# Performance work log

Hardware: AMD Instinct MI355X
Metric: run time of the kernel (lower is better)

## Reference

```python
import math
import jax, jax.numpy as jnp
import numpy as np

# ---------------- static config ----------------
L_MAX = 3
DIM = (L_MAX + 1) ** 2            # 16 = dim of 0e+1o+2e+3o
N_NODES = 8000
N_EDGES = 128000                  # avg 16 neighbors / node
F = 32                            # num_features (irrep multiplicity)
S = 10                            # num_species
NB = 8                            # num bessel basis fns
HID = 64                          # radial MLP hidden width
RD_HID = 16                       # readout MLP hidden (16x0e)
R_MAX = 5.0
AVG_NEIGH = 16.0
MEAN, STD = -1.5, 2.0
E0 = -10.0                        # atomic energy offset per node

_f = math.factorial

def _sl(l):
    return slice(l * l, (l + 1) * (l + 1))

# ---------------- real Clebsch-Gordan / Wigner-3j tables ----------------
def _su2_cg(j1, j2, j3):
    C = np.zeros((2 * j1 + 1, 2 * j2 + 1, 2 * j3 + 1))
    for m1 in range(-j1, j1 + 1):
        for m2 in range(-j2, j2 + 1):
            m3 = m1 + m2
            if abs(m3) > j3:
                continue
            pref = (2 * j3 + 1) * _f(j3 + j1 - j2) * _f(j3 - j1 + j2) * _f(j1 + j2 - j3) / _f(j1 + j2 + j3 + 1)
            pref *= _f(j3 + m3) * _f(j3 - m3) * _f(j1 - m1) * _f(j1 + m1) * _f(j2 - m2) * _f(j2 + m2)
            pref = math.sqrt(pref)
            s = 0.0
            for k in range(max(0, j2 - j3 - m1, j1 - j3 + m2), min(j1 + j2 - j3, j1 - m1, j2 + m2) + 1):
                s += (-1) ** k / (_f(k) * _f(j1 + j2 - j3 - k) * _f(j1 - m1 - k) * _f(j2 + m2 - k) * _f(j3 - j2 + m1 + k) * _f(j3 - j1 - m2 + k))
            C[j1 + m1, j2 + m2, j3 + m3] = pref * s
    return C

def _q_r2c(l):
    # complex <- real spherical-harmonic change of basis (e3nn convention)
    q = np.zeros((2 * l + 1, 2 * l + 1), dtype=complex)
    for m in range(-l, 0):
        q[l + m, l + abs(m)] = 1 / math.sqrt(2)
        q[l + m, l - abs(m)] = -1j / math.sqrt(2)
    q[l, l] = 1.0
    for m in range(1, l + 1):
        q[l + m, l + abs(m)] = (-1) ** m / math.sqrt(2)
        q[l + m, l - abs(m)] = 1j * (-1) ** m / math.sqrt(2)
    return (-1j) ** l * q

def _w3j(l1, l2, l3):
    C = _su2_cg(l1, l2, l3).astype(complex)
    C = np.einsum('abc,ai,bj,ck->ijk', C, _q_r2c(l1), _q_r2c(l2), np.conj(_q_r2c(l3)))
    assert np.abs(C.imag).max() < 1e-8
    return np.real(C)

PATHS = [(l1, l2, l3) for l1 in range(L_MAX + 1) for l2 in range(L_MAX + 1)
         for l3 in range(L_MAX + 1) if abs(l1 - l2) <= l3 <= l1 + l2]
NP_PATHS = len(PATHS)  # 34 CG paths
_W3J_NP = {p: _w3j(*p) for p in PATHS}
W3J = {p: jnp.asarray(v, dtype=jnp.float32) for p, v in _W3J_NP.items()}

def _sh_scales():
    # constants making recursively-built SH component-normalized (|Y_l|^2 = 2l+1)
    v = np.array([0.2, -0.6, 0.7]); v = v / np.linalg.norm(v)
    ys = {1: math.sqrt(3.0) * v}
    sc = {}
    for l in range(2, L_MAX + 1):
        t = np.einsum('abc,a,b->c', _W3J_NP[(l - 1, 1, l)], ys[l - 1], ys[1])
        sc[l] = math.sqrt(2 * l + 1) / np.linalg.norm(t)
        ys[l] = sc[l] * t
    return sc
SH_SCALE = _sh_scales()

# ---------------- equivariant building blocks ----------------
def spherical_harmonics(vectors):
    r = jnp.linalg.norm(vectors, axis=-1, keepdims=True)
    u = vectors / jnp.maximum(r, 1e-9)
    y1 = math.sqrt(3.0) * u
    Y = jnp.concatenate([jnp.ones_like(u[:, :1]), y1], axis=-1)
    prev = y1
    for l in range(2, L_MAX + 1):
        cur = SH_SCALE[l] * jnp.einsum('abc,ea,eb->ec', W3J[(l - 1, 1, l)], prev, y1)
        Y = jnp.concatenate([Y, cur], axis=-1)
        prev = cur
    return Y  # [E, 16]

def radial_embedding(r):
    # Bessel basis * polynomial envelope (RadialEmbeddingBlock)
    x = r / R_MAX
    n = jnp.arange(1, NB + 1, dtype=r.dtype)
    b = math.sqrt(2.0 / R_MAX) * jnp.sin(jnp.pi * x[:, None] * n[None, :]) / jnp.maximum(r, 1e-9)[:, None]
    p = 5.0
    env = 1 - (p + 1) * (p + 2) / 2 * x ** p + p * (p + 2) * x ** (p + 1) - p * (p + 1) / 2 * x ** (p + 2)
    env = jnp.where(x < 1.0, env, 0.0)
    return b * env[:, None]  # [E, NB]

def _lin(x, w):
    # e3nn Linear: per-l channel mixing. x [N,F,DIM], w [L_MAX+1,F,F]
    return jnp.concatenate([jnp.einsum('nfa,fg->nga', x[:, :, _sl(l)], w[l]) for l in range(L_MAX + 1)], axis=-1)

def _tp_edge(xs, Y, rw):
    # radially-weighted CG tensor product of node feats with edge SH (InteractionBlock core)
    out = jnp.zeros_like(xs)
    for p, (l1, l2, l3) in enumerate(PATHS):
        t = jnp.einsum('abc,efa,eb->efc', W3J[(l1, l2, l3)], xs[:, :, _sl(l1)], Y[:, _sl(l2)])
        out = out.at[:, :, _sl(l3)].add(rw[:, p, :, None] * t)
    return out

def _tp_node(x, y):
    # channel-wise symmetric CG product (EquivariantProductBasisBlock contraction)
    out = jnp.zeros_like(x)
    for (l1, l2, l3) in PATHS:
        t = jnp.einsum('abc,nfa,nfb->nfc', W3J[(l1, l2, l3)], x[:, :, _sl(l1)], y[:, :, _sl(l2)])
        out = out.at[:, :, _sl(l3)].add(t / math.sqrt(2 * l3 + 1))
    return out

# ---------------- inputs ----------------
def setup_inputs() -> dict:
    key = jax.random.key(0)
    ks = iter(jax.random.split(key, 40))
    def nrm(shape, fan):
        return jax.random.normal(next(ks), shape, dtype=jnp.float32) / math.sqrt(fan)
    inp = {}
    inp['vectors'] = jax.random.normal(next(ks), (N_EDGES, 3), dtype=jnp.float32) * 1.5
    inp['node_z'] = jax.random.randint(next(ks), (N_NODES,), 0, S)
    inp['senders'] = jax.random.randint(next(ks), (N_EDGES,), 0, N_NODES)
    inp['receivers'] = jax.random.randint(next(ks), (N_EDGES,), 0, N_NODES)
    inp['embed'] = nrm((S, F), 1)
    for i in (0, 1):
        inp['r%d_w0' % i] = nrm((NB, HID), NB)
        inp['r%d_w1' % i] = nrm((HID, HID), HID)
        inp['r%d_w2' % i] = nrm((HID, NP_PATHS * F), HID)
        inp['up%d' % i] = nrm((L_MAX + 1, F, F), F)
        inp['post%d' % i] = nrm((L_MAX + 1, F, F), F)
        inp['pb%d' % i] = nrm((S, 3, F), 1)
        inp['pblin%d' % i] = nrm((L_MAX + 1, F, F), F)
    inp['sel0'] = nrm((S, L_MAX + 1, F, F), F)
    inp['ro0'] = nrm((F, 1), F)
    inp['res1'] = nrm((S, F, F), F)
    inp['ro1_a'] = nrm((F, RD_HID), F)
    inp['ro1_b'] = nrm((RD_HID, 1), RD_HID)
    return inp

# ---------------- forward ----------------
def reference(vectors, node_z, senders, receivers, embed,
              r0_w0, r0_w1, r0_w2, up0, post0, pb0, pblin0, sel0, ro0,
              r1_w0, r1_w1, r1_w2, up1, post1, pb1, pblin1, res1, ro1_a, ro1_b):
    N = node_z.shape[0]
    r = jnp.linalg.norm(vectors, axis=-1)
    Y = spherical_harmonics(vectors)
    rad = radial_embedding(r)
    # node embedding: scalars only
    feats = jnp.zeros((N, F, DIM), vectors.dtype).at[:, :, 0].set(embed[node_z])

    def interaction(feats, w0, w1, w2, wup, wpost):
        h = _lin(feats, wup)
        rw = (jax.nn.silu(jax.nn.silu(rad @ w0) @ w1) @ w2).reshape(-1, NP_PATHS, F)
        msgs = _tp_edge(h[senders], Y, rw)
        agg = jax.ops.segment_sum(msgs, receivers, num_segments=N) / AVG_NEIGH
        return _lin(agg, wpost)

    def product_basis(A, wpb, wlin, z):
        B2 = _tp_node(A, A)           # correlation order 2
        B3 = _tp_node(B2, A)          # correlation order 3
        w = wpb[z]                     # [N,3,F] per-species contraction weights
        out = w[:, 0, :, None] * A + w[:, 1, :, None] * B2 + w[:, 2, :, None] * B3
        return _lin(out, wlin)

    # ---- layer 0: selector tensor product, linear readout ----
    h = interaction(feats, r0_w0, r0_w1, r0_w2, up0, post0)
    wz = sel0[node_z]  # FullyConnectedTensorProduct with one-hot species == per-species linear
    h = jnp.concatenate([jnp.einsum('nfa,nfg->nga', h[:, :, _sl(l)], wz[:, l]) for l in range(L_MAX + 1)], axis=-1)
    feats = product_basis(h, pb0, pblin0, node_z)
    e0 = (feats[:, :, 0] @ ro0)[:, 0]

    # ---- layer 1 (last): residual to scalars, nonlinear readout ----
    resid = jnp.einsum('nf,nfg->ng', feats[:, :, 0], res1[node_z])
    h = interaction(feats, r1_w0, r1_w1, r1_w2, up1, post1)
    h = product_basis(h, pb1, pblin1, node_z)
    sc = h[:, :, 0] + resid  # last-layer target irreps = F x 0e
    e1 = (jax.nn.silu(sc @ ro1_a) @ ro1_b)[:, 0]

    node_energies = MEAN + STD * (e0 + e1) + E0
    return jnp.sum(node_energies)
```

## Files before the change

kernel.cpp:

```cpp
#include <hip/hip_runtime.h>
#include <math.h>

#define NF 32
#define NPATHS 34

typedef __attribute__((ext_vector_type(8))) short bf16x8;
typedef __attribute__((ext_vector_type(4))) float f32x4;
typedef __attribute__((ext_vector_type(2))) float f32x2;

__device__ __forceinline__ unsigned short f2bf(float v){
  unsigned u = __float_as_uint(v);
  u += 0x7fffu + ((u>>16)&1u);
  return (unsigned short)(u>>16);
}
__device__ __forceinline__ float bf2f(unsigned short h){
  return __uint_as_float(((unsigned)h)<<16);
}

struct PathTab { int l1[NPATHS]; int l2[NPATHS]; int l3[NPATHS]; };
constexpr PathTab mkpaths(){
  PathTab t{}; int n=0;
  for(int a=0;a<=3;a++)for(int b=0;b<=3;b++)for(int c=0;c<=3;c++){
    int lo = a>b ? a-b : b-a;
    if(c>=lo && c<=a+b){ t.l1[n]=a; t.l2[n]=b; t.l3[n]=c; n++; }
  }
  return t;
}
constexpr PathTab PT = mkpaths();

struct FactT { double v[22]; };
constexpr FactT mkfactT(){ FactT f{}; f.v[0]=1.0; for(int i=1;i<22;i++) f.v[i]=f.v[i-1]*(double)i; return f; }
constexpr FactT FT = mkfactT();
constexpr double cfact(int n){ return FT.v[n]; }

constexpr double csqrt(double x){
  if(x<=0.0) return 0.0;
  double g = x<1.0 ? 1.0 : x;
  for(int i=0;i<40;i++) g=0.5*(g+x/g);
  return g;
}

constexpr double su2cg(int j1,int j2,int j3,int m1,int m2){
  int m3=m1+m2;
  if(m3<-j3||m3>j3) return 0.0;
  double pref = (double)(2*j3+1)*cfact(j3+j1-j2)*cfact(j3-j1+j2)*cfact(j1+j2-j3)/cfact(j1+j2+j3+1);
  pref *= cfact(j3+m3)*cfact(j3-m3)*cfact(j1-m1)*cfact(j1+m1)*cfact(j2-m2)*cfact(j2+m2);
  pref = csqrt(pref);
  int k0=0; if(j2-j3-m1>k0)k0=j2-j3-m1; if(j1-j3+m2>k0)k0=j1-j3+m2;
  int k1=j1+j2-j3; if(j1-m1<k1)k1=j1-m1; if(j2+m2<k1)k1=j2+m2;
  double s=0.0;
  for(int k=k0;k<=k1;k++){
    double d = cfact(k)*cfact(j1+j2-j3-k)*cfact(j1-m1-k)*cfact(j2+m2-k)*cfact(j3-j2+m1+k)*cfact(j3-j1-m2+k);
    s += (k&1)? -1.0/d : 1.0/d;
  }
  return pref*s;
}

struct ccd { double x, y; };
constexpr ccd cqval(int l,int r,int col){
  const double is2 = 0.70710678118654752440;
  double re=0.0, im=0.0;
  if (r<l){ if (col==2*l-r) re=is2; else if (col==r) im=-is2; }
  else if (r==l){ if (col==l) re=1.0; }
  else { double s = ((r-l)&1)? -1.0:1.0;
         if (col==r) re=s*is2; else if (col==2*l-r) im=s*is2; }
  ccd v{re,im};
  switch(l&3){
    case 1: return ccd{ v.y, -v.x };
    case 2: return ccd{-v.x, -v.y };
    case 3: return ccd{-v.y,  v.x };
    default: return v;
  }
}

constexpr double w3entry(int l1,int l2,int l3,int i,int j,int k){
  double re=0.0;
  for(int a=0;a<2*l1+1;a++){
    ccd qa=cqval(l1,a,i); if(qa.x==0.0&&qa.y==0.0) continue;
    for(int b=0;b<2*l2+1;b++){
      ccd qb=cqval(l2,b,j); if(qb.x==0.0&&qb.y==0.0) continue;
      int m1=a-l1, m2=b-l2, m3=m1+m2;
      if(m3<-l3||m3>l3) continue;
      int c=m3+l3;
      double cg=su2cg(l1,l2,l3,m1,m2); if(cg==0.0) continue;
      ccd qc=cqval(l3,c,k); qc.y=-qc.y;
      if(qc.x==0.0&&qc.y==0.0) continue;
      ccd ab{qa.x*qb.x-qa.y*qb.y, qa.x*qb.y+qa.y*qb.x};
      re += cg*(ab.x*qc.x - ab.y*qc.y);
    }
  }
  return re;
}

template<int L1,int L2,int L3> struct W3Arr { float v[(2*L1+1)*(2*L2+1)*(2*L3+1)]; };
template<int L1,int L2,int L3> constexpr W3Arr<L1,L2,L3> mkW3(double scale){
  W3Arr<L1,L2,L3> r{};
  for(int i=0;i<2*L1+1;i++)
    for(int j=0;j<2*L2+1;j++)
      for(int k=0;k<2*L3+1;k++)
        r.v[(i*(2*L2+1)+j)*(2*L3+1)+k] = (float)(w3entry(L1,L2,L3,i,j,k)*scale);
  return r;
}
template<int L1,int L2,int L3> constexpr W3Arr<L1,L2,L3> W3V = mkW3<L1,L2,L3>(1.0);
template<int L1,int L2,int L3> constexpr W3Arr<L1,L2,L3> W3N = mkW3<L1,L2,L3>(1.0/csqrt(2.0*L3+1.0));

struct SCt { double sc2, sc3; };
constexpr SCt mksc(){
  double v0=0.2,v1=-0.6,v2=0.7;
  double nv=csqrt(v0*v0+v1*v1+v2*v2);
  double s3=csqrt(3.0);
  double y1[3]={s3*v0/nv, s3*v1/nv, s3*v2/nv};
  double t2[5]={0,0,0,0,0}; double n2=0.0;
  for(int c=0;c<5;c++){
    double s=0.0;
    for(int a=0;a<3;a++)for(int b=0;b<3;b++) s += w3entry(1,1,2,a,b,c)*y1[a]*y1[b];
    t2[c]=s; n2+=s*s;
  }
  double sc2=csqrt(5.0)/csqrt(n2);
  double y2[5]={sc2*t2[0],sc2*t2[1],sc2*t2[2],sc2*t2[3],sc2*t2[4]};
  double n3=0.0;
  for(int c=0;c<7;c++){
    double s=0.0;
    for(int a=0;a<5;a++)for(int b=0;b<3;b++) s += w3entry(2,1,3,a,b,c)*y2[a]*y1[b];
    n3+=s*s;
  }
  double sc3=csqrt(7.0)/csqrt(n3);
  return SCt{sc2,sc3};
}
constexpr SCt SCV = mksc();

template<bool NORM,int l1,int l2,int l3,int A,int B,int C>
__device__ __forceinline__ void w3term(const float* __restrict__ x, const float* __restrict__ y,
                                       float rv, float* __restrict__ acc){
  constexpr float w = NORM ? W3N<l1,l2,l3>.v[(A*(2*l2+1)+B)*(2*l3+1)+C]
                           : W3V<l1,l2,l3>.v[(A*(2*l2+1)+B)*(2*l3+1)+C];
  if constexpr (w!=0.0f)
    acc[l3*l3+C] = fmaf(w, x[l1*l1+A]*y[l2*l2+B]*rv, acc[l3*l3+C]);
}
template<bool NORM,int l1,int l2,int l3,int A,int B,int C>
__device__ __forceinline__ void w3loopC(const float* x,const float* y,float rv,float* acc){
  if constexpr (C<2*l3+1){
    w3term<NORM,l1,l2,l3,A,B,C>(x,y,rv,acc);
    w3loopC<NORM,l1,l2,l3,A,B,C+1>(x,y,rv,acc);
  }
}
template<bool NORM,int l1,int l2,int l3,int A,int B>
__device__ __forceinline__ void w3loopB(const float* x,const float* y,float rv,float* acc){
  if constexpr (B<2*l2+1){
    w3loopC<NORM,l1,l2,l3,A,B,0>(x,y,rv,acc);
    w3loopB<NORM,l1,l2,l3,A,B+1>(x,y,rv,acc);
  }
}
template<bool NORM,int l1,int l2,int l3,int A>
__device__ __forceinline__ void w3loopA(const float* x,const float* y,float rv,float* acc){
  if constexpr (A<2*l1+1){
    w3loopB<NORM,l1,l2,l3,A,0>(x,y,rv,acc);
    w3loopA<NORM,l1,l2,l3,A+1>(x,y,rv,acc);
  }
}

template<int P>
__device__ __forceinline__ void tpn_paths(const float* x,const float* y,float* o){
  if constexpr (P<NPATHS){
    constexpr int l1=PT.l1[P], l2=PT.l2[P], l3=PT.l3[P];
    w3loopA<true,l1,l2,l3,0>(x,y,1.0f,o);
    tpn_paths<P+1>(x,y,o);
  }
}

__device__ __forceinline__ float tpn_scalar(const float* x,const float* y){
  float o[1]={0.f};
  w3loopA<true,0,0,0,0>(x,y,1.0f,o);
  w3loopA<true,1,1,0,0>(x,y,1.0f,o);
  w3loopA<true,2,2,0,0>(x,y,1.0f,o);
  w3loopA<true,3,3,0,0>(x,y,1.0f,o);
  return o[0];
}

template<int l1,int l2,int l3,int A,int B>
constexpr bool anyNZ(){
  for(int c=0;c<2*l3+1;c++)
    if(W3V<l1,l2,l3>.v[(A*(2*l2+1)+B)*(2*l3+1)+c]!=0.0f) return true;
  return false;
}
template<int l1,int l2,int l3,int A,int B,int C>
__device__ __forceinline__ void w3C2(const f32x2 p, f32x2* __restrict__ S){
  constexpr float w = W3V<l1,l2,l3>.v[(A*(2*l2+1)+B)*(2*l3+1)+C];
  if constexpr (w!=0.0f) S[C] = p*w + S[C];
  if constexpr (C+1<2*l3+1) w3C2<l1,l2,l3,A,B,C+1>(p,S);
}
template<int l1,int l2,int l3,int A,int B>
__device__ __forceinline__ void w3B2(const f32x2* __restrict__ x,const f32x2* __restrict__ y,
                                     f32x2* __restrict__ S){
  if constexpr (anyNZ<l1,l2,l3,A,B>()){
    f32x2 p = x[l1*l1+A]*y[l2*l2+B];
    w3C2<l1,l2,l3,A,B,0>(p,S);
  }
  if constexpr (B+1<2*l2+1) w3B2<l1,l2,l3,A,B+1>(x,y,S);
}
template<int l1,int l2,int l3,int A>
__device__ __forceinline__ void w3A2(const f32x2* __restrict__ x,const f32x2* __restrict__ y,
                                     f32x2* __restrict__ S){
  w3B2<l1,l2,l3,A,0>(x,y,S);
  if constexpr (A+1<2*l1+1) w3A2<l1,l2,l3,A+1>(x,y,S);
}
template<bool L0,int P>
__device__ __forceinline__ void tp2(const f32x2* __restrict__ x,const f32x2* __restrict__ y,
                                    const unsigned short* __restrict__ rpA,
                                    const unsigned short* __restrict__ rpB,
                                    f32x2* __restrict__ acc){
  if constexpr (P<NPATHS){
    constexpr int l1=PT.l1[P], l2=PT.l2[P], l3=PT.l3[P];
    if constexpr (!(L0 && l1!=0)){
      f32x2 S[2*l3+1];
      #pragma unroll
      for(int c=0;c<2*l3+1;c++) S[c]=(f32x2){0.f,0.f};
      w3A2<l1,l2,l3,0>(x,y,S);
      f32x2 rv = { bf2f(rpA[P]), bf2f(rpB[P]) };
      #pragma unroll
      for(int c=0;c<2*l3+1;c++) acc[l3*l3+c] = rv*S[c] + acc[l3*l3+c];
    }
    tp2<L0,P+1>(x,y,rpA,rpB,acc);
  }
}

__global__ __launch_bounds__(256) void k_count(
    const int* __restrict__ rcv, int* __restrict__ deg, int E)
{
  int e=blockIdx.x*256+threadIdx.x;
  if(e>=E) return;
  atomicAdd(&deg[rcv[e]],1);
}

#define SCAN_PER 32
__global__ __launch_bounds__(1024) void k_scan(
    const int* __restrict__ deg, int* __restrict__ row,
    int* __restrict__ cur, int N)
{
  __shared__ int part[1024];
  int t=threadIdx.x;
  int per=(N+1023)/1024; if(per>SCAN_PER) per=SCAN_PER;
  int base=t*per;
  int loc[SCAN_PER];
  int s=0;
  for(int i=0;i<per;i++){ int idx=base+i; int v=(idx<N)? deg[idx]:0; loc[i]=s; s+=v; }
  part[t]=s;
  __syncthreads();
  for(int off=1;off<1024;off<<=1){
    int v=(t>=off)? part[t-off]:0;
    __syncthreads();
    part[t]+=v;
    __syncthreads();
  }
  int ex=(t==0)?0:part[t-1];
  for(int i=0;i<per;i++){
    int idx=base+i;
    if(idx<N){ int r=ex+loc[i]; row[idx]=r; cur[idx]=r; }
  }
  if(t==1023) row[N]=part[1023];
}

__global__ __launch_bounds__(256) void k_fill(
    const int* __restrict__ rcv, int* __restrict__ cur,
    int* __restrict__ eid, int E)
{
  int e=blockIdx.x*256+threadIdx.x;
  if(e>=E) return;
  int pos=atomicAdd(&cur[rcv[e]],1);
  eid[pos]=e;
}

__global__ __launch_bounds__(256) void k_edge_setup(
    const float* __restrict__ vec, const int* __restrict__ snd,
    const int* __restrict__ eid, float* __restrict__ Y,
    float* __restrict__ rad, int* __restrict__ snd_s, int E)
{
  int j = blockIdx.x*256+threadIdx.x;
  if (j>=E) return;
  int e = eid[j];
  snd_s[j]=snd[e];
  float vx=vec[3*e], vy=vec[3*e+1], vz=vec[3*e+2];
  float r=sqrtf(vx*vx+vy*vy+vz*vz);
  float inv=1.0f/fmaxf(r,1e-9f);
  float y[16];
  y[0]=1.0f;
  const float s3=1.7320508075688772f;
  y[1]=s3*vx*inv; y[2]=s3*vy*inv; y[3]=s3*vz*inv;
  constexpr float sc2=(float)SCV.sc2, sc3=(float)SCV.sc3;
  {
    float t[16];
    #pragma unroll
    for(int c=0;c<16;c++) t[c]=0.f;
    w3loopA<false,1,1,2,0>(y,y,1.0f,t);
    #pragma unroll
    for(int c=0;c<5;c++) y[4+c]=sc2*t[4+c];
    w3loopA<false,2,1,3,0>(y,y,1.0f,t);
    #pragma unroll
    for(int c=0;c<7;c++) y[9+c]=sc3*t[9+c];
  }
  float4* Yp=(float4*)(Y+(size_t)j*16);
  Yp[0]=make_float4(y[0],y[1],y[2],y[3]);
  Yp[1]=make_float4(y[4],y[5],y[6],y[7]);
  Yp[2]=make_float4(y[8],y[9],y[10],y[11]);
  Yp[3]=make_float4(y[12],y[13],y[14],y[15]);
  float x = r*0.2f;
  float env=0.f;
  if (x<1.0f){
    float x2=x*x; float x4=x2*x2; float x5=x4*x;
    env = 1.0f - 21.0f*x5 + 35.0f*x5*x - 15.0f*x5*x2;
  }
  const float cb = 0.632455532033675866f;
  float base = inv*env*cb;
  #pragma unroll
  for(int n=1;n<=8;n++)
    rad[(size_t)j*8 + n-1] = base*sinf(3.14159265358979323846f * x * (float)n);
}

__global__ __launch_bounds__(256) void k_embed16(
    const float* __restrict__ embed, const float* __restrict__ up0,
    const int* __restrict__ z, unsigned short* __restrict__ hl16, int N)
{
  int t=blockIdx.x*256+threadIdx.x;
  int n=t>>5, g=t&31;
  if(n>=N) return;
  const float* ep=embed+z[n]*32;
  float a=0.f;
  #pragma unroll 8
  for(int f=0;f<32;f++) a=fmaf(ep[f],up0[(f<<5)+g],a);
  bf16x8 o0={(short)f2bf(a),0,0,0,0,0,0,0};
  bf16x8 o1={0,0,0,0,0,0,0,0};
  bf16x8* op=(bf16x8*)(hl16+(size_t)n*512+g*16);
  op[0]=o0; op[1]=o1;
}

__global__ __launch_bounds__(256) void k_radial(
    const float* __restrict__ rad, const float* __restrict__ w0,
    const float* __restrict__ w1, unsigned short* __restrict__ hid, int E)
{
  __shared__ float w0s[8*64];
  __shared__ float w1s[64*64];
  int tid=threadIdx.x;
  for(int i=tid;i<512;i+=256) w0s[i]=w0[i];
  for(int i=tid;i<4096;i+=256) w1s[i]=w1[i];
  __syncthreads();
  int e=blockIdx.x*256+tid;
  if(e>=E) return;
  const float4* rp=(const float4*)(rad+(size_t)e*8);
  float4 ra=rp[0], rb=rp[1];
  float rv[8]={ra.x,ra.y,ra.z,ra.w,rb.x,rb.y,rb.z,rb.w};
  float h1[64];
  #pragma unroll 8
  for(int j=0;j<64;j++){
    float a=0.f;
    #pragma unroll
    for(int i=0;i<8;i++) a=fmaf(rv[i],w0s[i*64+j],a);
    h1[j]=a/(1.f+__expf(-a));
  }
  unsigned short* hp = hid+(size_t)e*64;
  #pragma unroll 4
  for(int j=0;j<64;j++){
    float a=0.f;
    #pragma unroll
    for(int i=0;i<64;i++) a=fmaf(h1[i],w1s[i*64+j],a);
    hp[j]=f2bf(a/(1.f+__expf(-a)));
  }
}

__global__ __launch_bounds__(256) void k_prep(
    const float* __restrict__ w2a, const float* __restrict__ w2b,
    unsigned short* __restrict__ ta, unsigned short* __restrict__ tb,
    const float* __restrict__ post0, const float* __restrict__ sel0,
    float* __restrict__ comb)
{
  int t=blockIdx.x*256+threadIdx.x;
  const int C2=2*1088*64;
  if(t<C2){
    const float* src = (t<1088*64)? w2a : w2b;
    unsigned short* dst = (t<1088*64)? ta : tb;
    int u = (t<1088*64)? t : t-1088*64;
    int c=u>>6, k=u&63;
    dst[(size_t)c*64+k]=f2bf(src[(size_t)k*1088+c]);
  } else {
    int u=t-C2;
    if(u<10*4096){
      int z=u>>12, r=u&4095;
      int l=r>>10, e=(r>>5)&31, g=r&31;
      const float* pp=post0+l*1024+e*32;
      const float* sp=sel0+(size_t)z*4096+l*1024;
      float a=0.f;
      #pragma unroll 8
      for(int f=0;f<32;f++) a=fmaf(pp[f], sp[f*32+g], a);
      comb[(size_t)z*4096 + l*1024 + e*32 + g]=a;
    }
  }
}

template<bool L0>
__global__ __launch_bounds__(256,3) void k_tp_fused(
    const unsigned short* __restrict__ hlin, const float* __restrict__ Y,
    const unsigned short* __restrict__ hid, const unsigned short* __restrict__ w2t,
    const int* __restrict__ snd_s, unsigned short* __restrict__ msgs,
    int eb, int ecnt)
{
  constexpr int NT  = L0 ? 8 : 68;
  constexpr int FS  = L0 ? 4 : 36;
  constexpr int ROW = 32*FS + 4;
  __shared__ unsigned short rws[16*ROW] __attribute__((aligned(16)));
  int tid=threadIdx.x;
  int lane=tid&63, wave=tid>>6;
  int m16=lane&15, quad=lane>>4;
  int el0=blockIdx.x*16;
  int f=tid&31;
  int hb=(tid>>5)&1;
  int le0 = wave + hb*8;
  int le1 = le0 + 4;
  int elA = el0 + le0, elB = el0 + le1;
  bool okA = elA<ecnt, okB = elB<ecnt;
  int sA = okA ? snd_s[eb+elA] : 0;
  int sB = okB ? snd_s[eb+elB] : 0;
  {
    const unsigned short* Ab = hid + (size_t)el0*64;
    bf16x8 a0 = *(const bf16x8*)(Ab + m16*64 + quad*8);
    bf16x8 a1 = *(const bf16x8*)(Ab + m16*64 + 32 + quad*8);
    #pragma unroll 4
    for(int nt=wave; nt<NT; nt+=4){
      int col = nt*16 + m16;
      bf16x8 b0 = *(const bf16x8*)(w2t + (size_t)col*64 + quad*8);
      bf16x8 b1 = *(const bf16x8*)(w2t + (size_t)col*64 + 32 + quad*8);
      f32x4 acc = (f32x4){0.f,0.f,0.f,0.f};
      acc = __builtin_amdgcn_mfma_f32_16x16x32_bf16(a0,b0,acc,0,0,0);
      acc = __builtin_amdgcn_mfma_f32_16x16x32_bf16(a1,b1,acc,0,0,0);
      int fo=(col&31)*FS + (col>>5);
      #pragma unroll
      for(int r=0;r<4;r++)
        rws[(quad*4+r)*ROW + fo] = f2bf(acc[r]);
    }
  }
  __syncthreads();
  if(!okA) return;
  int jA = eb+elA;
  int jB = okB ? eb+elB : jA;
  const unsigned short* rpA = rws + le0*ROW + f*FS;
  const unsigned short* rpB = rws + le1*ROW + f*FS;
  f32x2 hs[16];
  if constexpr (L0){
    const unsigned short* hA = hlin + (size_t)sA*512 + f*16;
    const unsigned short* hB = hlin + (size_t)sB*512 + f*16;
    hs[0] = (f32x2){ bf2f(hA[0]), bf2f(hB[0]) };
  } else {
    const bf16x8* hA = (const bf16x8*)(hlin + (size_t)sA*512 + f*16);
    const bf16x8* hB = (const bf16x8*)(hlin + (size_t)sB*512 + f*16);
    bf16x8 ha0=hA[0], ha1=hA[1], hb0=hB[0], hb1=hB[1];
    #pragma unroll
    for(int c=0;c<8;c++){
      hs[c]   = (f32x2){ bf2f((unsigned short)ha0[c]), bf2f((unsigned short)hb0[c]) };
      hs[8+c] = (f32x2){ bf2f((unsigned short)ha1[c]), bf2f((unsigned short)hb1[c]) };
    }
  }
  f32x2 yv[16];
  {
    const float4* yA=(const float4*)(Y+(size_t)jA*16);
    const float4* yB=(const float4*)(Y+(size_t)jB*16);
    float4 a0=yA[0],a1=yA[1],a2=yA[2],a3=yA[3];
    float4 b0=yB[0],b1=yB[1],b2=yB[2],b3=yB[3];
    yv[0]=(f32x2){a0.x,b0.x}; yv[1]=(f32x2){a0.y,b0.y}; yv[2]=(f32x2){a0.z,b0.z}; yv[3]=(f32x2){a0.w,b0.w};
    yv[4]=(f32x2){a1.x,b1.x}; yv[5]=(f32x2){a1.y,b1.y}; yv[6]=(f32x2){a1.z,b1.z}; yv[7]=(f32x2){a1.w,b1.w};
    yv[8]=(f32x2){a2.x,b2.x}; yv[9]=(f32x2){a2.y,b2.y}; yv[10]=(f32x2){a2.z,b2.z}; yv[11]=(f32x2){a2.w,b2.w};
    yv[12]=(f32x2){a3.x,b3.x}; yv[13]=(f32x2){a3.y,b3.y}; yv[14]=(f32x2){a3.z,b3.z}; yv[15]=(f32x2){a3.w,b3.w};
  }
  f32x2 acc[16];
  #pragma unroll
  for(int c=0;c<16;c++) acc[c]=(f32x2){0.f,0.f};
  tp2<L0,0>(hs,yv,rpA,rpB,acc);
  {
    bf16x8 m0, m1;
    #pragma unroll
    for(int c=0;c<8;c++){
      m0[c]=(short)f2bf(acc[c].x*0.0625f);
      m1[c]=(short)f2bf(acc[8+c].x*0.0625f);
    }
    bf16x8* mp=(bf16x8*)(msgs+(size_t)elA*512+f*16);
    mp[0]=m0; mp[1]=m1;
  }
  if(okB){
    bf16x8 m0, m1;
    #pragma unroll
    for(int c=0;c<8;c++){
      m0[c]=(short)f2bf(acc[c].y*0.0625f);
      m1[c]=(short)f2bf(acc[8+c].y*0.0625f);
    }
    bf16x8* mp=(bf16x8*)(msgs+(size_t)elB*512+f*16);
    mp[0]=m0; mp[1]=m1;
  }
}

template<bool INIT>
__global__ __launch_bounds__(256) void k_seg_sum(
    const unsigned short* __restrict__ msgs, const int* __restrict__ row,
    float* __restrict__ agg, int eb, int ecnt, int N)
{
  int t=blockIdx.x*256+threadIdx.x;
  int n=t>>6, q=t&63;
  if(n>=N) return;
  int lo=row[n], hi=row[n+1];
  int a0 = lo>eb ? lo : eb;
  int a1e = eb+ecnt;
  int a1 = hi<a1e ? hi : a1e;
  if(!INIT && a0>=a1) return;
  float s[8];
  #pragma unroll
  for(int i=0;i<8;i++) s[i]=0.f;
  for(int j=a0;j<a1;j++){
    bf16x8 v=*(const bf16x8*)(msgs+(size_t)(j-eb)*512+q*8);
    #pragma unroll
    for(int i=0;i<8;i++) s[i]+=bf2f((unsigned short)v[i]);
  }
  float4* a0p=(float4*)(agg+(size_t)n*512+q*8);
  if(INIT){
    a0p[0]=make_float4(s[0],s[1],s[2],s[3]);
    a0p[1]=make_float4(s[4],s[5],s[6],s[7]);
  } else {
    float4 o0=a0p[0], o1=a0p[1];
    o0.x+=s[0]; o0.y+=s[1]; o0.z+=s[2]; o0.w+=s[3];
    o1.x+=s[4]; o1.y+=s[5]; o1.z+=s[6]; o1.w+=s[7];
    a0p[0]=o0; a0p[1]=o1;
  }
}

__global__ __launch_bounds__(256) void k_node0(
    const float* __restrict__ agg, const float* __restrict__ combw,
    const float* __restrict__ pb0, const float* __restrict__ pblin0,
    const float* __restrict__ ro0, const float* __restrict__ res1,
    const float* __restrict__ up1, const int* __restrict__ z,
    float* __restrict__ e0, float* __restrict__ resid,
    unsigned short* __restrict__ hl16, int N)
{
  __shared__ float sh1[8*512] __attribute__((aligned(16)));
  __shared__ float sh2[8*512] __attribute__((aligned(16)));
  int tid=threadIdx.x;
  int n0=tid>>5, g=tid&31;
  int n=blockIdx.x*8+n0;
  bool act=(n<N);
  int zz = act? z[n] : 0;
  if(act){
    const float* wp = combw + (size_t)zz*4096;
    const float* ip = agg + (size_t)n*512;
    float A[16];
    #pragma unroll
    for(int c=0;c<16;c++) A[c]=0.f;
    #pragma unroll 8
    for(int f=0;f<NF;f++){
      const float4* xp=(const float4*)(ip+f*16);
      float4 x0=xp[0],x1=xp[1],x2=xp[2],x3=xp[3];
      float w0v=wp[(f<<5)+g],w1v=wp[1024+(f<<5)+g],w2v=wp[2048+(f<<5)+g],w3v=wp[3072+(f<<5)+g];
      A[0]=fmaf(x0.x,w0v,A[0]);  A[1]=fmaf(x0.y,w1v,A[1]);  A[2]=fmaf(x0.z,w1v,A[2]);  A[3]=fmaf(x0.w,w1v,A[3]);
      A[4]=fmaf(x1.x,w2v,A[4]);  A[5]=fmaf(x1.y,w2v,A[5]);  A[6]=fmaf(x1.z,w2v,A[6]);  A[7]=fmaf(x1.w,w2v,A[7]);
      A[8]=fmaf(x2.x,w2v,A[8]);  A[9]=fmaf(x2.y,w3v,A[9]);  A[10]=fmaf(x2.z,w3v,A[10]);A[11]=fmaf(x2.w,w3v,A[11]);
      A[12]=fmaf(x3.x,w3v,A[12]);A[13]=fmaf(x3.y,w3v,A[13]);A[14]=fmaf(x3.z,w3v,A[14]);A[15]=fmaf(x3.w,w3v,A[15]);
    }
    float B2[16],B3[16];
    #pragma unroll
    for(int c=0;c<16;c++){ B2[c]=0.f; B3[c]=0.f; }
    tpn_paths<0>(A,A,B2);
    tpn_paths<0>(B2,A,B3);
    float wa=pb0[zz*96+g], wb=pb0[zz*96+32+g], wc=pb0[zz*96+64+g];
    #pragma unroll
    for(int c=0;c<16;c++) sh1[n0*512+g*16+c]=wa*A[c]+wb*B2[c]+wc*B3[c];
  }
  __syncthreads();
  if(act){
    float ft[16];
    #pragma unroll
    for(int c=0;c<16;c++) ft[c]=0.f;
    const float* wp=pblin0;
    #pragma unroll 8
    for(int f=0;f<NF;f++){
      const float4* xp=(const float4*)(sh1+n0*512+f*16);
      float4 x0=xp[0],x1=xp[1],x2=xp[2],x3=xp[3];
      float w0v=wp[(f<<5)+g],w1v=wp[1024+(f<<5)+g],w2v=wp[2048+(f<<5)+g],w3v=wp[3072+(f<<5)+g];
      ft[0]=fmaf(x0.x,w0v,ft[0]);  ft[1]=fmaf(x0.y,w1v,ft[1]);  ft[2]=fmaf(x0.z,w1v,ft[2]);  ft[3]=fmaf(x0.w,w1v,ft[3]);
      ft[4]=fmaf(x1.x,w2v,ft[4]);  ft[5]=fmaf(x1.y,w2v,ft[5]);  ft[6]=fmaf(x1.z,w2v,ft[6]);  ft[7]=fmaf(x1.w,w2v,ft[7]);
      ft[8]=fmaf(x2.x,w2v,ft[8]);  ft[9]=fmaf(x2.y,w3v,ft[9]);  ft[10]=fmaf(x2.z,w3v,ft[10]);ft[11]=fmaf(x2.w,w3v,ft[11]);
      ft[12]=fmaf(x3.x,w3v,ft[12]);ft[13]=fmaf(x3.y,w3v,ft[13]);ft[14]=fmaf(x3.z,w3v,ft[14]);ft[15]=fmaf(x3.w,w3v,ft[15]);
    }
    #pragma unroll
    for(int c=0;c<16;c++) sh2[n0*512+g*16+c]=ft[c];
  }
  __syncthreads();
  if(act){
    const float* wp=res1+(size_t)zz*1024;
    float a=0.f;
    #pragma unroll 8
    for(int f=0;f<32;f++) a=fmaf(sh2[n0*512+f*16], wp[(f<<5)+g], a);
    resid[(size_t)n*32+g]=a;
    if(g==0){
      float b=0.f;
      #pragma unroll 8
      for(int f=0;f<32;f++) b=fmaf(sh2[n0*512+f*16], ro0[f], b);
      e0[n]=b;
    }
    float acc[16];
    #pragma unroll
    for(int c=0;c<16;c++) acc[c]=0.f;
    const float* wp2=up1;
    #pragma unroll 8
    for(int f=0;f<NF;f++){
      const float4* xp=(const float4*)(sh2+n0*512+f*16);
      float4 x0=xp[0],x1=xp[1],x2=xp[2],x3=xp[3];
      float w0v=wp2[(f<<5)+g],w1v=wp2[1024+(f<<5)+g],w2v=wp2[2048+(f<<5)+g],w3v=wp2[3072+(f<<5)+g];
      acc[0]=fmaf(x0.x,w0v,acc[0]);  acc[1]=fmaf(x0.y,w1v,acc[1]);  acc[2]=fmaf(x0.z,w1v,acc[2]);  acc[3]=fmaf(x0.w,w1v,acc[3]);
      acc[4]=fmaf(x1.x,w2v,acc[4]);  acc[5]=fmaf(x1.y,w2v,acc[5]);  acc[6]=fmaf(x1.z,w2v,acc[6]);  acc[7]=fmaf(x1.w,w2v,acc[7]);
      acc[8]=fmaf(x2.x,w2v,acc[8]);  acc[9]=fmaf(x2.y,w3v,acc[9]);  acc[10]=fmaf(x2.z,w3v,acc[10]);acc[11]=fmaf(x2.w,w3v,acc[11]);
      acc[12]=fmaf(x3.x,w3v,acc[12]);acc[13]=fmaf(x3.y,w3v,acc[13]);acc[14]=fmaf(x3.z,w3v,acc[14]);acc[15]=fmaf(x3.w,w3v,acc[15]);
    }
    bf16x8 o0,o1;
    #pragma unroll
    for(int c=0;c<8;c++){ o0[c]=(short)f2bf(acc[c]); o1[c]=(short)f2bf(acc[8+c]); }
    bf16x8* op=(bf16x8*)(hl16+(size_t)n*512+g*16);
    op[0]=o0; op[1]=o1;
  }
}

__global__ __launch_bounds__(256) void k_node1(
    const float* __restrict__ agg, const float* __restrict__ post1,
    const float* __restrict__ pb1, const float* __restrict__ pblin1,
    const int* __restrict__ z, const float* __restrict__ resid,
    const float* __restrict__ e0a, const float* __restrict__ ro1a,
    const float* __restrict__ ro1b, float* __restrict__ out, int N)
{
  __shared__ float sh[8*32];
  __shared__ float sh2[8*32];
  __shared__ float red[8];
  int tid=threadIdx.x;
  int n0=tid>>5, g=tid&31;
  int n=blockIdx.x*8+n0;
  bool act=(n<N);
  if(act){
    const float* wp=post1;
    const float* ip=agg+(size_t)n*512;
    float A[16];
    #pragma unroll
    for(int c=0;c<16;c++) A[c]=0.f;
    #pragma unroll 8
    for(int f=0;f<NF;f++){
      const float4* xp=(const float4*)(ip+f*16);
      float4 x0=xp[0],x1=xp[1],x2=xp[2],x3=xp[3];
      float w0v=wp[(f<<5)+g],w1v=wp[1024+(f<<5)+g],w2v=wp[2048+(f<<5)+g],w3v=wp[3072+(f<<5)+g];
      A[0]=fmaf(x0.x,w0v,A[0]);  A[1]=fmaf(x0.y,w1v,A[1]);  A[2]=fmaf(x0.z,w1v,A[2]);  A[3]=fmaf(x0.w,w1v,A[3]);
      A[4]=fmaf(x1.x,w2v,A[4]);  A[5]=fmaf(x1.y,w2v,A[5]);  A[6]=fmaf(x1.z,w2v,A[6]);  A[7]=fmaf(x1.w,w2v,A[7]);
      A[8]=fmaf(x2.x,w2v,A[8]);  A[9]=fmaf(x2.y,w3v,A[9]);  A[10]=fmaf(x2.z,w3v,A[10]);A[11]=fmaf(x2.w,w3v,A[11]);
      A[12]=fmaf(x3.x,w3v,A[12]);A[13]=fmaf(x3.y,w3v,A[13]);A[14]=fmaf(x3.z,w3v,A[14]);A[15]=fmaf(x3.w,w3v,A[15]);
    }
    float B2[16];
    #pragma unroll
    for(int c=0;c<16;c++) B2[c]=0.f;
    tpn_paths<0>(A,A,B2);
    float B3_0=tpn_scalar(B2,A);
    int zz=z[n];
    float wa=pb1[zz*96+g], wb=pb1[zz*96+32+g], wc=pb1[zz*96+64+g];
    sh[n0*32+g]=wa*A[0]+wb*B2[0]+wc*B3_0;
  }
  __syncthreads();
  if(act){
    float a=0.f;
    #pragma unroll 8
    for(int f=0;f<32;f++) a=fmaf(sh[n0*32+f], pblin1[(f<<5)+g], a);
    sh2[n0*32+g]=a+resid[(size_t)n*32+g];
  }
  __syncthreads();
  if(g==0){
    float val=0.f;
    if(act){
      float e1=0.f;
      #pragma unroll
      for(int j=0;j<16;j++){
        float a=0.f;
        #pragma unroll
        for(int f=0;f<32;f++) a=fmaf(sh2[n0*32+f],ro1a[f*16+j],a);
        float s=a/(1.f+__expf(-a));
        e1=fmaf(s,ro1b[j],e1);
      }
      val=-1.5f+2.0f*(e0a[n]+e1)-10.0f;
    }
    red[n0]=val;
  }
  __syncthreads();
  if(tid==0){
    float s=0.f;
    #pragma unroll
    for(int i=0;i<8;i++) s+=red[i];
    atomicAdd(out,s);
  }
}

extern "C" void kernel_launch(void* const* d_in, const int* in_sizes, int n_in,
                              void* d_out, int out_size, void* d_ws, size_t ws_size,
                              hipStream_t stream)
{
  const float* vec   =(const float*)d_in[0];
  const int*   zarr  =(const int*)  d_in[1];
  const int*   snd   =(const int*)  d_in[2];
  const int*   rcv   =(const int*)  d_in[3];
  const float* embed =(const float*)d_in[4];
  const float* r0w0  =(const float*)d_in[5];
  const float* r0w1  =(const float*)d_in[6];
  const float* r0w2  =(const float*)d_in[7];
  const float* up0   =(const float*)d_in[8];
  const float* post0 =(const float*)d_in[9];
  const float* pb0   =(const float*)d_in[10];
  const float* pblin0=(const float*)d_in[11];
  const float* r1w0  =(const float*)d_in[12];
  const float* r1w1  =(const float*)d_in[13];
  const float* r1w2  =(const float*)d_in[14];
  const float* up1   =(const float*)d_in[15];
  const float* post1 =(const float*)d_in[16];
  const float* pb1   =(const float*)d_in[17];
  const float* pblin1=(const float*)d_in[18];
  const float* sel0  =(const float*)d_in[19];
  const float* ro0   =(const float*)d_in[20];
  const float* res1  =(const float*)d_in[21];
  const float* ro1a  =(const float*)d_in[22];
  const float* ro1b  =(const float*)d_in[23];

  const int E = in_sizes[0]/3;
  const int N = in_sizes[1];
  const int Epad = (E+63)&~63;

  char* ws=(char*)d_ws;
  size_t o=0;
  auto alloc=[&](size_t bytes)->char*{
    char* p=ws+o;
    o=(o+bytes+255)&~(size_t)255;
    return p;
  };
  int*   deg  =(int*)  alloc((size_t)N*4);
  int*   rowp =(int*)  alloc((size_t)(N+1)*4);
  int*   cur  =(int*)  alloc((size_t)N*4);
  int*   eid  =(int*)  alloc((size_t)E*4);
  int*   snd_s=(int*)  alloc((size_t)E*4);
  float* Yb   =(float*)alloc((size_t)E*16*4);
  float* radb =(float*)alloc((size_t)E*8*4);
  unsigned short* hidb=(unsigned short*)alloc((size_t)(Epad+16)*64*2);
  unsigned short* w2t0=(unsigned short*)alloc((size_t)1088*64*2);
  unsigned short* w2t1=(unsigned short*)alloc((size_t)1088*64*2);
  unsigned short* hl16=(unsigned short*)alloc((size_t)N*512*2);
  float* combw=(float*)alloc((size_t)10*4096*4);
  float* bufB =(float*)alloc((size_t)N*512*4);
  float* bufC =(float*)alloc((size_t)N*512*4);
  float* e0b  =(float*)alloc((size_t)N*4);
  float* residb=(float*)alloc((size_t)N*32*4);
  char*  dyn  = ws+o;
  size_t remain = ws_size>o ? ws_size-o : 0;

  dim3 tb(256);
  dim3 nblk((unsigned)((N*32+255)/256));
  dim3 n8blk((unsigned)((N+7)/8));
  dim3 eblk((unsigned)((E+255)/256));
  dim3 qblk((unsigned)((N*64+255)/256));

  hipMemsetAsync(deg,0,(size_t)N*4,stream);
  k_count<<<eblk,tb,0,stream>>>(rcv,deg,E);
  k_scan<<<dim3(1),dim3(1024),0,stream>>>(deg,rowp,cur,N);
  k_fill<<<eblk,tb,0,stream>>>(rcv,cur,eid,E);

  k_edge_setup<<<eblk,tb,0,stream>>>(vec,snd,eid,Yb,radb,snd_s,E);
  k_prep<<<dim3((2*1088*64+10*4096+255)/256),tb,0,stream>>>(r0w2,r1w2,w2t0,w2t1,post0,sel0,combw);
  k_embed16<<<nblk,tb,0,stream>>>(embed,up0,zarr,hl16,N);

  auto run_edges=[&](bool l0, const unsigned short* hlin, const unsigned short* w2t, float* agg){
    long rows = (long)(remain/1024);
    rows -= rows%64;
    if (rows>(long)Epad) rows=Epad;
    if (rows<64) rows=64;
    unsigned short* msgsb = (unsigned short*)dyn;
    for(long eb=0;eb<E;eb+=rows){
      long cnt = E-eb; if(cnt>rows) cnt=rows;
      dim3 g2((unsigned)((cnt+15)/16));
      if(l0) k_tp_fused<true ><<<g2,tb,0,stream>>>(hlin,Yb,hidb+(size_t)eb*64,w2t,snd_s,msgsb,(int)eb,(int)cnt);
      else   k_tp_fused<false><<<g2,tb,0,stream>>>(hlin,Yb,hidb+(size_t)eb*64,w2t,snd_s,msgsb,(int)eb,(int)cnt);
      if(eb==0) k_seg_sum<true ><<<qblk,tb,0,stream>>>(msgsb,rowp,agg,(int)eb,(int)cnt,N);
      else      k_seg_sum<false><<<qblk,tb,0,stream>>>(msgsb,rowp,agg,(int)eb,(int)cnt,N);
    }
  };

  k_radial<<<eblk,tb,0,stream>>>(radb,r0w0,r0w1,hidb,E);
  run_edges(true,hl16,w2t0,bufB);
  k_node0<<<n8blk,tb,0,stream>>>(bufB,combw,pb0,pblin0,ro0,res1,up1,zarr,e0b,residb,hl16,N);

  k_radial<<<eblk,tb,0,stream>>>(radb,r1w0,r1w1,hidb,E);
  run_edges(false,hl16,w2t1,bufC);
  hipMemsetAsync(d_out,0,4,stream);
  k_node1<<<n8blk,tb,0,stream>>>(bufC,post1,pb1,pblin1,zarr,residb,e0b,ro1a,ro1b,(float*)d_out,N);
}
```

Baseline: 615.9 us.

## Give each wave a private LDS strip of radial weights, removing block barrier

The edge-block kernel is reorganised so each wave computes, via MFMA, only the radial weights for its own 8-feature slice across all 16 edges. It stores them in a wave-private LDS strip and then does the tensor product for those features. This removes the __syncthreads between the GEMM and TP phases and changes LDS padding. Each wave now issues MFMAs for half-discarded tiles, since only the lanes whose column half matches the wave parity store results. The occupancy hint in launch_bounds is also dropped.

Result: slower. 794.3 us (+29.0%).

```diff
diff --git a/kernel.cpp b/kernel.cpp
--- a/kernel.cpp
+++ b/kernel.cpp
@@ -396,57 +396,58 @@
 }
 
 template<bool L0>
-__global__ __launch_bounds__(256,3) void k_tp_fused(
+__global__ __launch_bounds__(256) void k_tp_fused(
     const unsigned short* __restrict__ hlin, const float* __restrict__ Y,
     const unsigned short* __restrict__ hid, const unsigned short* __restrict__ w2t,
     const int* __restrict__ snd_s, unsigned short* __restrict__ msgs,
     int eb, int ecnt)
 {
-  constexpr int NT  = L0 ? 8 : 68;
+  constexpr int NP  = L0 ? 4 : 34;
   constexpr int FS  = L0 ? 4 : 36;
-  constexpr int ROW = 32*FS + 4;
-  __shared__ unsigned short rws[16*ROW] __attribute__((aligned(16)));
+  constexpr int ESTR= L0 ? 34 : 294;
+  __shared__ unsigned short rws[4*16*ESTR] __attribute__((aligned(16)));
   int tid=threadIdx.x;
   int lane=tid&63, wave=tid>>6;
   int m16=lane&15, quad=lane>>4;
   int el0=blockIdx.x*16;
-  int f=tid&31;
-  int hb=(tid>>5)&1;
-  int le0 = wave + hb*8;
-  int le1 = le0 + 4;
-  int elA = el0 + le0, elB = el0 + le1;
-  bool okA = elA<ecnt, okB = elB<ecnt;
-  int sA = okA ? snd_s[eb+elA] : 0;
-  int sB = okB ? snd_s[eb+elB] : 0;
+  unsigned short* wstrip = rws + wave*(16*ESTR);
+
   {
     const unsigned short* Ab = hid + (size_t)el0*64;
     bf16x8 a0 = *(const bf16x8*)(Ab + m16*64 + quad*8);
     bf16x8 a1 = *(const bf16x8*)(Ab + m16*64 + 32 + quad*8);
+    bool act = ((m16>>3) == (wave&1));
+    int fi = m16 & 7;
+    int fh = wave>>1;
+    unsigned short* wp = wstrip + quad*4*ESTR + fi*FS;
     #pragma unroll 4
-    for(int nt=wave; nt<NT; nt+=4){
-      int col = nt*16 + m16;
-      bf16x8 b0 = *(const bf16x8*)(w2t + (size_t)col*64 + quad*8);
-      bf16x8 b1 = *(const bf16x8*)(w2t + (size_t)col*64 + 32 + quad*8);
+    for(int p=0;p<NP;p++){
+      int col = (2*p+fh)*16 + m16;
+      const unsigned short* Bp = w2t + (size_t)col*64;
+      bf16x8 b0 = *(const bf16x8*)(Bp + quad*8);
+      bf16x8 b1 = *(const bf16x8*)(Bp + 32 + quad*8);
       f32x4 acc = (f32x4){0.f,0.f,0.f,0.f};
       acc = __builtin_amdgcn_mfma_f32_16x16x32_bf16(a0,b0,acc,0,0,0);
       acc = __builtin_amdgcn_mfma_f32_16x16x32_bf16(a1,b1,acc,0,0,0);
-      int fo=(col&31)*FS + (col>>5);
-      #pragma unroll
-      for(int r=0;r<4;r++)
-        rws[(quad*4+r)*ROW + fo] = f2bf(acc[r]);
-    }
-  }
-  __syncthreads();
-  if(!okA) return;
-  int jA = eb+elA;
-  int jB = okB ? eb+elB : jA;
-  const unsigned short* rpA = rws + le0*ROW + f*FS;
-  const unsigned short* rpB = rws + le1*ROW + f*FS;
+      if(act){
+        #pragma unroll
+        for(int r=0;r<4;r++) wp[r*ESTR + p] = f2bf(acc[r]);
+      }
+    }
+  }
+
+  int fi2 = lane&7, j = lane>>3;
+  int f = wave*8 + fi2;
+  int elA = el0 + j, elB = el0 + j + 8;
+  bool okA = elA<ecnt, okB = elB<ecnt;
+  int sA = okA ? snd_s[eb+elA] : 0;
+  int sB = okB ? snd_s[eb+elB] : 0;
+  size_t jA = okA ? (size_t)(eb+elA) : 0;
+  size_t jB = okB ? (size_t)(eb+elB) : 0;
   f32x2 hs[16];
   if constexpr (L0){
-    const unsigned short* hA = hlin + (size_t)sA*512 + f*16;
-    const unsigned short* hB = hlin + (size_t)sB*512 + f*16;
-    hs[0] = (f32x2){ bf2f(hA[0]), bf2f(hB[0]) };
+    hs[0] = (f32x2){ bf2f(hlin[(size_t)sA*512 + f*16]),
+                     bf2f(hlin[(size_t)sB*512 + f*16]) };
   } else {
     const bf16x8* hA = (const bf16x8*)(hlin + (size_t)sA*512 + f*16);
     const bf16x8* hB = (const bf16x8*)(hlin + (size_t)sB*512 + f*16);
@@ -459,8 +460,8 @@
   }
   f32x2 yv[16];
   {
-    const float4* yA=(const float4*)(Y+(size_t)jA*16);
-    const float4* yB=(const float4*)(Y+(size_t)jB*16);
+    const float4* yA=(const float4*)(Y+jA*16);
+    const float4* yB=(const float4*)(Y+jB*16);
     float4 a0=yA[0],a1=yA[1],a2=yA[2],a3=yA[3];
     float4 b0=yB[0],b1=yB[1],b2=yB[2],b3=yB[3];
     yv[0]=(f32x2){a0.x,b0.x}; yv[1]=(f32x2){a0.y,b0.y}; yv[2]=(f32x2){a0.z,b0.z}; yv[3]=(f32x2){a0.w,b0.w};
@@ -468,11 +469,13 @@
     yv[8]=(f32x2){a2.x,b2.x}; yv[9]=(f32x2){a2.y,b2.y}; yv[10]=(f32x2){a2.z,b2.z}; yv[11]=(f32x2){a2.w,b2.w};
     yv[12]=(f32x2){a3.x,b3.x}; yv[13]=(f32x2){a3.y,b3.y}; yv[14]=(f32x2){a3.z,b3.z}; yv[15]=(f32x2){a3.w,b3.w};
   }
+  const unsigned short* rpA = wstrip + j*ESTR + fi2*FS;
+  const unsigned short* rpB = wstrip + (j+8)*ESTR + fi2*FS;
   f32x2 acc[16];
   #pragma unroll
   for(int c=0;c<16;c++) acc[c]=(f32x2){0.f,0.f};
   tp2<L0,0>(hs,yv,rpA,rpB,acc);
-  {
+  if(okA){
     bf16x8 m0, m1;
     #pragma unroll
     for(int c=0;c<8;c++){
```

## Split fused radial GEMM and tensor product into separate kernels via global buffer

Applied to the files above, without the earlier changes.

Splits the fused kernel into an MFMA GEMM that writes per-edge radial weights to a global buffer and a streaming tensor-product kernel that reads them. This drops the shared-memory staging and block barrier, which limited occupancy. In exchange it adds a large global write and read of the radial weights per edge, and chunks get smaller because the workspace must also hold that buffer.

Result: slower. 748.4 us (+21.5%).

```diff
diff --git a/kernel.cpp b/kernel.cpp
--- a/kernel.cpp
+++ b/kernel.cpp
@@ -206,8 +206,8 @@
 }
 template<bool L0,int P>
 __device__ __forceinline__ void tp2(const f32x2* __restrict__ x,const f32x2* __restrict__ y,
-                                    const unsigned short* __restrict__ rpA,
-                                    const unsigned short* __restrict__ rpB,
+                                    const unsigned short* __restrict__ rA,
+                                    const unsigned short* __restrict__ rB,
                                     f32x2* __restrict__ acc){
   if constexpr (P<NPATHS){
     constexpr int l1=PT.l1[P], l2=PT.l2[P], l3=PT.l3[P];
@@ -216,11 +216,11 @@
       #pragma unroll
       for(int c=0;c<2*l3+1;c++) S[c]=(f32x2){0.f,0.f};
       w3A2<l1,l2,l3,0>(x,y,S);
-      f32x2 rv = { bf2f(rpA[P]), bf2f(rpB[P]) };
+      f32x2 rv = { bf2f(rA[P*32]), bf2f(rB[P*32]) };
       #pragma unroll
       for(int c=0;c<2*l3+1;c++) acc[l3*l3+c] = rv*S[c] + acc[l3*l3+c];
     }
-    tp2<L0,P+1>(x,y,rpA,rpB,acc);
+    tp2<L0,P+1>(x,y,rA,rB,acc);
   }
 }
 
@@ -396,57 +396,55 @@
 }
 
 template<bool L0>
-__global__ __launch_bounds__(256,3) void k_tp_fused(
-    const unsigned short* __restrict__ hlin, const float* __restrict__ Y,
+__global__ __launch_bounds__(256) void k_rwgemm(
     const unsigned short* __restrict__ hid, const unsigned short* __restrict__ w2t,
-    const int* __restrict__ snd_s, unsigned short* __restrict__ msgs,
-    int eb, int ecnt)
-{
-  constexpr int NT  = L0 ? 8 : 68;
-  constexpr int FS  = L0 ? 4 : 36;
-  constexpr int ROW = 32*FS + 4;
-  __shared__ unsigned short rws[16*ROW] __attribute__((aligned(16)));
+    unsigned short* __restrict__ rwg, int ecnt)
+{
+  constexpr int NT = L0 ? 8 : 68;
+  constexpr int NC = L0 ? 128 : 1088;
   int tid=threadIdx.x;
   int lane=tid&63, wave=tid>>6;
   int m16=lane&15, quad=lane>>4;
   int el0=blockIdx.x*16;
-  int f=tid&31;
-  int hb=(tid>>5)&1;
-  int le0 = wave + hb*8;
-  int le1 = le0 + 4;
-  int elA = el0 + le0, elB = el0 + le1;
-  bool okA = elA<ecnt, okB = elB<ecnt;
-  int sA = okA ? snd_s[eb+elA] : 0;
-  int sB = okB ? snd_s[eb+elB] : 0;
-  {
-    const unsigned short* Ab = hid + (size_t)el0*64;
-    bf16x8 a0 = *(const bf16x8*)(Ab + m16*64 + quad*8);
-    bf16x8 a1 = *(const bf16x8*)(Ab + m16*64 + 32 + quad*8);
-    #pragma unroll 4
-    for(int nt=wave; nt<NT; nt+=4){
-      int col = nt*16 + m16;
-      bf16x8 b0 = *(const bf16x8*)(w2t + (size_t)col*64 + quad*8);
-      bf16x8 b1 = *(const bf16x8*)(w2t + (size_t)col*64 + 32 + quad*8);
-      f32x4 acc = (f32x4){0.f,0.f,0.f,0.f};
-      acc = __builtin_amdgcn_mfma_f32_16x16x32_bf16(a0,b0,acc,0,0,0);
-      acc = __builtin_amdgcn_mfma_f32_16x16x32_bf16(a1,b1,acc,0,0,0);
-      int fo=(col&31)*FS + (col>>5);
-      #pragma unroll
-      for(int r=0;r<4;r++)
-        rws[(quad*4+r)*ROW + fo] = f2bf(acc[r]);
-    }
-  }
-  __syncthreads();
-  if(!okA) return;
-  int jA = eb+elA;
-  int jB = okB ? eb+elB : jA;
-  const unsigned short* rpA = rws + le0*ROW + f*FS;
-  const unsigned short* rpB = rws + le1*ROW + f*FS;
+  const unsigned short* Ab = hid + (size_t)el0*64;
+  bf16x8 a0 = *(const bf16x8*)(Ab + m16*64 + quad*8);
+  bf16x8 a1 = *(const bf16x8*)(Ab + m16*64 + 32 + quad*8);
+  int erow = el0 + quad*4;
+  #pragma unroll 4
+  for(int nt=wave; nt<NT; nt+=4){
+    int col = nt*16 + m16;
+    bf16x8 b0 = *(const bf16x8*)(w2t + (size_t)col*64 + quad*8);
+    bf16x8 b1 = *(const bf16x8*)(w2t + (size_t)col*64 + 32 + quad*8);
+    f32x4 acc = (f32x4){0.f,0.f,0.f,0.f};
+    acc = __builtin_amdgcn_mfma_f32_16x16x32_bf16(a0,b0,acc,0,0,0);
+    acc = __builtin_amdgcn_mfma_f32_16x16x32_bf16(a1,b1,acc,0,0,0);
+    #pragma unroll
+    for(int r=0;r<4;r++)
+      rwg[(size_t)(erow+r)*NC + col] = f2bf(acc[r]);
+  }
+}
+
+template<bool L0>
+__global__ __launch_bounds__(256) void k_tp_stream(
+    const unsigned short* __restrict__ hlin, const float* __restrict__ Y,
+    const unsigned short* __restrict__ rwg, const int* __restrict__ snd_s,
+    unsigned short* __restrict__ msgs, int eb, int ecnt)
+{
+  constexpr int NC = L0 ? 128 : 1088;
+  int T = blockIdx.x*256 + threadIdx.x;
+  int f = T & 31;
+  int q = T >> 5;
+  int eA = 2*q, eB = 2*q+1;
+  if (eA >= ecnt) return;
+  bool okB = (eB < ecnt);
+  int sA = snd_s[eb+eA];
+  int sB = okB ? snd_s[eb+eB] : sA;
+  size_t jA = (size_t)(eb+eA);
+  size_t jB = okB ? (size_t)(eb+eB) : jA;
   f32x2 hs[16];
   if constexpr (L0){
-    const unsigned short* hA = hlin + (size_t)sA*512 + f*16;
-    const unsigned short* hB = hlin + (size_t)sB*512 + f*16;
-    hs[0] = (f32x2){ bf2f(hA[0]), bf2f(hB[0]) };
+    hs[0] = (f32x2){ bf2f(hlin[(size_t)sA*512 + f*16]),
+                     bf2f(hlin[(size_t)sB*512 + f*16]) };
   } else {
     const bf16x8* hA = (const bf16x8*)(hlin + (size_t)sA*512 + f*16);
     const bf16x8* hB = (const bf16x8*)(hlin + (size_t)sB*512 + f*16);
@@ -459,8 +457,8 @@
   }
   f32x2 yv[16];
   {
-    const float4* yA=(const float4*)(Y+(size_t)jA*16);
-    const float4* yB=(const float4*)(Y+(size_t)jB*16);
+    const float4* yA=(const float4*)(Y+jA*16);
+    const float4* yB=(const float4*)(Y+jB*16);
     float4 a0=yA[0],a1=yA[1],a2=yA[2],a3=yA[3];
     float4 b0=yB[0],b1=yB[1],b2=yB[2],b3=yB[3];
     yv[0]=(f32x2){a0.x,b0.x}; yv[1]=(f32x2){a0.y,b0.y}; yv[2]=(f32x2){a0.z,b0.z}; yv[3]=(f32x2){a0.w,b0.w};
@@ -468,10 +466,12 @@
     yv[8]=(f32x2){a2.x,b2.x}; yv[9]=(f32x2){a2.y,b2.y}; yv[10]=(f32x2){a2.z,b2.z}; yv[11]=(f32x2){a2.w,b2.w};
     yv[12]=(f32x2){a3.x,b3.x}; yv[13]=(f32x2){a3.y,b3.y}; yv[14]=(f32x2){a3.z,b3.z}; yv[15]=(f32x2){a3.w,b3.w};
   }
+  const unsigned short* rA = rwg + (size_t)eA*NC + f;
+  const unsigned short* rB = rwg + (size_t)(okB?eB:eA)*NC + f;
   f32x2 acc[16];
   #pragma unroll
   for(int c=0;c<16;c++) acc[c]=(f32x2){0.f,0.f};
-  tp2<L0,0>(hs,yv,rpA,rpB,acc);
+  tp2<L0,0>(hs,yv,rA,rB,acc);
   {
     bf16x8 m0, m1;
     #pragma unroll
@@ -479,7 +479,7 @@
       m0[c]=(short)f2bf(acc[c].x*0.0625f);
       m1[c]=(short)f2bf(acc[8+c].x*0.0625f);
     }
-    bf16x8* mp=(bf16x8*)(msgs+(size_t)elA*512+f*16);
+    bf16x8* mp=(bf16x8*)(msgs+(size_t)eA*512+f*16);
     mp[0]=m0; mp[1]=m1;
   }
   if(okB){
@@ -489,7 +489,7 @@
       m0[c]=(short)f2bf(acc[c].y*0.0625f);
       m1[c]=(short)f2bf(acc[8+c].y*0.0625f);
     }
-    bf16x8* mp=(bf16x8*)(msgs+(size_t)elB*512+f*16);
+    bf16x8* mp=(bf16x8*)(msgs+(size_t)eB*512+f*16);
     mp[0]=m0; mp[1]=m1;
   }
 }
@@ -768,16 +768,24 @@
   k_embed16<<<nblk,tb,0,stream>>>(embed,up0,zarr,hl16,N);
 
   auto run_edges=[&](bool l0, const unsigned short* hlin, const unsigned short* w2t, float* agg){
-    long rows = (long)(remain/1024);
+    const long NCl = l0 ? 128 : 1088;
+    long per = NCl*2 + 1024;
+    long rows = (long)(remain/per);
     rows -= rows%64;
     if (rows>(long)Epad) rows=Epad;
     if (rows<64) rows=64;
-    unsigned short* msgsb = (unsigned short*)dyn;
+    unsigned short* rwgb  = (unsigned short*)dyn;
+    unsigned short* msgsb = (unsigned short*)(dyn + (size_t)rows*NCl*2);
     for(long eb=0;eb<E;eb+=rows){
       long cnt = E-eb; if(cnt>rows) cnt=rows;
       dim3 g2((unsigned)((cnt+15)/16));
-      if(l0) k_tp_fused<true ><<<g2,tb,0,stream>>>(hlin,Yb,hidb+(size_t)eb*64,w2t,snd_s,msgsb,(int)eb,(int)cnt);
-      else   k_tp_fused<false><<<g2,tb,0,stream>>>(hlin,Yb,hidb+(size_t)eb*64,w2t,snd_s,msgsb,(int)eb,(int)cnt);
+      if(l0){
+        k_rwgemm <true ><<<g2,tb,0,stream>>>(hidb+(size_t)eb*64,w2t,rwgb,(int)cnt);
+        k_tp_stream<true ><<<g2,tb,0,stream>>>(hlin,Yb,rwgb,snd_s,msgsb,(int)eb,(int)cnt);
+      } else {
+        k_rwgemm <false><<<g2,tb,0,stream>>>(hidb+(size_t)eb*64,w2t,rwgb,(int)cnt);
+        k_tp_stream<false><<<g2,tb,0,stream>>>(hlin,Yb,rwgb,snd_s,msgsb,(int)eb,(int)cnt);
+      }
       if(eb==0) k_seg_sum<true ><<<qblk,tb,0,stream>>>(msgsb,rowp,agg,(int)eb,(int)cnt,N);
       else      k_seg_sum<false><<<qblk,tb,0,stream>>>(msgsb,rowp,agg,(int)eb,(int)cnt,N);
     }
```
